# Kernel optimization log

Measured on AMD Instinct MI355X. Metric: run time of the kernel, lower is better.

## Reference

```python
import jax, jax.numpy as jnp
import numpy as np

B, N, D = 32, 256, 3
NF, L = 16, 3


def _fully_connected(n):
    # Same ordering as connect_fully: for i in range(n) for j in range(n) if i != j
    a = np.repeat(np.arange(n), n)
    b = np.tile(np.arange(n), n)
    m = a != b
    return a[m].astype(np.int32), b[m].astype(np.int32)


def setup_inputs() -> dict:
    key = jax.random.key(0)
    ks = jax.random.split(key, 12)
    src, dst = _fully_connected(N)
    s = 0.1  # small param scale for numerical stability
    return {
        "xs": jax.random.normal(ks[0], (B, N, D), jnp.float32),
        "vs": jax.random.normal(ks[1], (B, N, D), jnp.float32),
        "charges": jax.random.normal(ks[2], (B * N, 1), jnp.float32),
        "W_in": s * jax.random.normal(ks[3], (1, NF), jnp.float32),
        "b_in": jnp.zeros((NF,), jnp.float32),
        "W_v": s * jax.random.normal(ks[4], (L, NF, 1), jnp.float32),
        "We1": s * jax.random.normal(ks[5], (L, 2 * NF + 1, NF), jnp.float32),
        "be1": jnp.zeros((L, NF), jnp.float32),
        "We2": s * jax.random.normal(ks[6], (L, NF, NF), jnp.float32),
        "be2": jnp.zeros((L, NF), jnp.float32),
        "Wx": s * jax.random.normal(ks[7], (L, NF, 1), jnp.float32),
        "Wh1": s * jax.random.normal(ks[8], (L, 2 * NF, NF), jnp.float32),
        "bh1": jnp.zeros((L, NF), jnp.float32),
        "src": jnp.asarray(src),
        "dst": jnp.asarray(dst),
    }


def reference(xs, vs, charges, W_in, b_in, W_v, We1, be1, We2, be2, Wx, Wh1, bh1, src, dst):
    b, n, d = xs.shape
    # node scalar features from charges (ndata['f'])
    h = jax.nn.relu(charges.reshape(b, n, 1) @ W_in + b_in)  # [B,N,nf]
    x = xs
    n_layers = We1.shape[0]
    for l in range(n_layers):
        # fully-connected edge gather + subtract (edata['d'])
        de = x[:, dst] - x[:, src]                         # [B,E,3]
        r2 = jnp.sum(de * de, axis=-1, keepdims=True)      # [B,E,1]
        e_in = jnp.concatenate([h[:, src], h[:, dst], r2], axis=-1)  # [B,E,2nf+1]
        m = jax.nn.relu(e_in @ We1[l] + be1[l])
        m = jax.nn.relu(m @ We2[l] + be2[l])               # [B,E,nf]
        w = m @ Wx[l]                                      # [B,E,1]
        # equivariant coordinate update: scatter-add edge vectors into dst nodes
        agg_x = jnp.zeros_like(x).at[:, dst].add(de * w) / (n - 1)
        x = x + agg_x + vs * (h @ W_v[l])                  # velocity term (ndata['vel'])
        m_agg = jnp.zeros_like(h).at[:, dst].add(m)        # [B,N,nf]
        h = h + jax.nn.relu(jnp.concatenate([h, m_agg], axis=-1) @ Wh1[l] + bh1[l])
    # OurDynamics returns (se3_out['1'] + xs).view(-1, n_dimension)
    return x.reshape(-1, d)
```

## Files before the change

kernel.cpp:

```cpp
#include <hip/hip_runtime.h>

#define NN 256
#define NF 16

typedef _Float16 half4 __attribute__((ext_vector_type(4)));
typedef _Float16 h2 __attribute__((ext_vector_type(2)));
typedef __fp16 fh2 __attribute__((ext_vector_type(2)));
typedef float f32x4 __attribute__((ext_vector_type(4)));

#define CVTPK(a, b) __builtin_bit_cast(h2, __builtin_amdgcn_cvt_pkrtz((a), (b)))
#define FDOT2(a, b, c) __builtin_amdgcn_fdot2(__builtin_bit_cast(fh2, (a)), __builtin_bit_cast(fh2, (b)), (c), false)

#define XA_OFF 0
#define XB_OFF 32768
#define HA_OFF 65536
#define HB_OFF 196608
#define SUA_OFF 327680
#define SVA_OFF 458752
#define SUB_OFF 589824
#define SVB_OFF 720896

__global__ __launch_bounds__(256)
void layer0_kernel(const float* __restrict__ xs, const float* __restrict__ vs,
                   const float* __restrict__ charges,
                   const float* __restrict__ W_in, const float* __restrict__ b_in,
                   const float* __restrict__ W_v, const float* __restrict__ We1_l,
                   const float* __restrict__ be1_l, const float* __restrict__ We2_l,
                   const float* __restrict__ be2_l, const float* __restrict__ Wx_l,
                   const float* __restrict__ Wh1_l, const float* __restrict__ bh1_l,
                   const float* __restrict__ We1_n, const float* __restrict__ be1_n,
                   float* __restrict__ x_out, float* __restrict__ h_out,
                   float* __restrict__ su_out, float* __restrict__ sv_out) {
    __shared__ __align__(16) _Float16 sSUh[NN][20];
    __shared__ __align__(16) float sX[NN * 4];
    __shared__ __align__(16) float sHg[64 * NF];
    __shared__ float sWs[256], sWd[256];
    __shared__ __align__(16) float sSV8[8][NF];
    __shared__ __align__(16) float sH8[8][NF + 1];
    __shared__ float sWh1s[512];
    __shared__ float sWa[256], sWb[256];
    __shared__ float sbe1n[NF];
    __shared__ float sh_new[8][NF + 1];
    __shared__ float sg[8][NF];

    const int tid  = threadIdx.x;
    const int b    = blockIdx.x >> 5;
    const int oct  = blockIdx.x & 31;
    const int n0l  = 8 * oct;
    const size_t n0 = (size_t)b * NN + n0l;
    const int w    = tid >> 6;
    const int lane = tid & 63;
    const int c    = lane & 15;
    const int g    = lane >> 4;

    sWs[tid] = We1_l[tid];
    sWd[tid] = We1_l[256 + tid];
    sWh1s[tid]       = Wh1_l[tid];
    sWh1s[256 + tid] = Wh1_l[256 + tid];
    {
        const int f = tid >> 4, kk = tid & 15;
        sWa[kk * NF + f] = We1_n[tid];
        sWb[kk * NF + f] = We1_n[256 + tid];
        if (tid < NF) sbe1n[tid] = be1_n[tid];
    }
    {
        const size_t base = ((size_t)b * NN + tid) * 3;
        const float x0v = xs[base + 0], x1v = xs[base + 1], x2v = xs[base + 2];
        sX[tid * 4 + 0] = x0v;
        sX[tid * 4 + 1] = x1v;
        sX[tid * 4 + 2] = x2v;
        sX[tid * 4 + 3] = fmaf(x0v, x0v, fmaf(x1v, x1v, x2v * x2v));
    }

    const int nl = tid >> 4, k = tid & 15;
    const float win  = W_in[k];
    const float bin  = b_in[k];
    const float be1k = be1_l[k];
    const int i0 = n0l >> 6;
    const int r0 = (n0l & 63) >> 4;
    const int halfsel = (n0l >> 3) & 1;
    const int own = ((nl >> 3) == halfsel);
#pragma unroll
    for (int i = 0; i < 4; ++i) {
#pragma unroll
        for (int r = 0; r < 4; ++r) {
            const float cq = charges[(size_t)b * NN + 64 * i + 16 * r + nl];
            const float hf = fmaxf(fmaf(cq, win, bin), 0.f);
            sHg[(16 * r + nl) * NF + k] = hf;
            if (i == i0 && r == r0 && own) sH8[nl & 7][k] = hf;
        }
        __syncthreads();
#pragma unroll
        for (int r = 0; r < 4; ++r) {
            const float4* hn = (const float4*)&sHg[(16 * r + nl) * NF];
            const float4 h0q = hn[0], h1q = hn[1], h2q = hn[2], h3q = hn[3];
            float u = 0.f;
#pragma unroll
            for (int q = 0; q < 4; ++q) {
                const float4 hq = (q == 0) ? h0q : (q == 1) ? h1q : (q == 2) ? h2q : h3q;
                u = fmaf(hq.x, sWs[(4 * q + 0) * NF + k], u);
                u = fmaf(hq.y, sWs[(4 * q + 1) * NF + k], u);
                u = fmaf(hq.z, sWs[(4 * q + 2) * NF + k], u);
                u = fmaf(hq.w, sWs[(4 * q + 3) * NF + k], u);
            }
            sSUh[64 * i + 16 * r + nl][k] = (_Float16)u;
            if (i == i0 && r == r0 && own) {
                float v = be1k;
#pragma unroll
                for (int q = 0; q < 4; ++q) {
                    const float4 hq = (q == 0) ? h0q : (q == 1) ? h1q : (q == 2) ? h2q : h3q;
                    v = fmaf(hq.x, sWd[(4 * q + 0) * NF + k], v);
                    v = fmaf(hq.y, sWd[(4 * q + 1) * NF + k], v);
                    v = fmaf(hq.z, sWd[(4 * q + 2) * NF + k], v);
                    v = fmaf(hq.w, sWd[(4 * q + 3) * NF + k], v);
                }
                sSV8[nl & 7][k] = v;
            }
        }
        __syncthreads();
    }

    const int j0 = n0l + w, j1 = n0l + 4 + w;
    const float4 xj0 = *(const float4*)&sX[4 * j0];
    const float4 xj1 = *(const float4*)&sX[4 * j1];
    half4 afrag;
    afrag.x = (_Float16)We2_l[(4 * g + 0) * NF + c];
    afrag.y = (_Float16)We2_l[(4 * g + 1) * NF + c];
    afrag.z = (_Float16)We2_l[(4 * g + 2) * NF + c];
    afrag.w = (_Float16)We2_l[(4 * g + 3) * NF + c];
    const float4 v40 = *(const float4*)&sSV8[w][4 * g];
    const float4 v41 = *(const float4*)&sSV8[4 + w][4 * g];
    const float4 wr4  = *(const float4*)(We1_l + 512 + 4 * g);
    const float4 be2f = *(const float4*)(be2_l + 4 * g);
    const float4 wxf  = *(const float4*)(Wx_l + 4 * g);
    f32x4 cb;
    cb.x = be2f.x; cb.y = be2f.y; cb.z = be2f.z; cb.w = be2f.w;
    const h2 wrp01 = CVTPK(wr4.x, wr4.y), wrp23 = CVTPK(wr4.z, wr4.w);
    const h2 vp001 = CVTPK(v40.x, v40.y), vp023 = CVTPK(v40.z, v40.w);
    const h2 vp101 = CVTPK(v41.x, v41.y), vp123 = CVTPK(v41.z, v41.w);
    const h2 wxp01 = CVTPK(wxf.x, wxf.y), wxp23 = CVTPK(wxf.z, wxf.w);
    h2 hz; hz.x = (_Float16)0.f; hz.y = (_Float16)0.f;
    const float m20x = -2.f * xj0.x, m20y = -2.f * xj0.y, m20z = -2.f * xj0.z;
    const float m21x = -2.f * xj1.x, m21y = -2.f * xj1.y, m21z = -2.f * xj1.z;

    float Sw0 = 0.f, Swx0 = 0.f, Swy0 = 0.f, Swz0 = 0.f;
    float Sw1 = 0.f, Swx1 = 0.f, Swy1 = 0.f, Swz1 = 0.f;
    h2 g01_0 = hz, g23_0 = hz, g01_1 = hz, g23_1 = hz;

    const _Float16* su_lh = &sSUh[c][4 * g];
    const float* x_l  = &sX[4 * c];

#pragma unroll 2
    for (int t = 0; t < 16; ++t) {
        const half4 uh = *(const half4*)(su_lh + 320 * t);
        const float4 xs4 = *(const float4*)(x_l + 64 * t);
        h2 u01, u23;
        u01.x = uh.x; u01.y = uh.y; u23.x = uh.z; u23.y = uh.w;
        const int s = 16 * t + c;
        {
            const float r2 = fmaf(m20x, xs4.x, fmaf(m20y, xs4.y, fmaf(m20z, xs4.z, xs4.w + xj0.w)));
            const h2 r2v = CVTPK(r2, r2);
            const h2 m01 = __builtin_elementwise_max(r2v * wrp01 + (u01 + vp001), hz);
            const h2 m23 = __builtin_elementwise_max(r2v * wrp23 + (u23 + vp023), hz);
            half4 bfrag;
            bfrag.x = m01.x; bfrag.y = m01.y; bfrag.z = m23.x; bfrag.w = m23.y;
            const f32x4 acc = __builtin_amdgcn_mfma_f32_16x16x16f16(afrag, bfrag, cb, 0, 0, 0);
            const h2 e01 = __builtin_elementwise_max(CVTPK(acc.x, acc.y), hz);
            const h2 e23 = __builtin_elementwise_max(CVTPK(acc.z, acc.w), hz);
            const float wp = FDOT2(e01, wxp01, FDOT2(e23, wxp23, 0.f));
            const unsigned gm = (s != j0) ? 0x3C003C00u : 0u;
            const h2 gu = __builtin_bit_cast(h2, gm);
            g01_0 = e01 * gu + g01_0;
            g23_0 = e23 * gu + g23_0;
            Sw0 += wp;
            Swx0 = fmaf(wp, xs4.x, Swx0);
            Swy0 = fmaf(wp, xs4.y, Swy0);
            Swz0 = fmaf(wp, xs4.z, Swz0);
        }
        {
            const float r2 = fmaf(m21x, xs4.x, fmaf(m21y, xs4.y, fmaf(m21z, xs4.z, xs4.w + xj1.w)));
            const h2 r2v = CVTPK(r2, r2);
            const h2 m01 = __builtin_elementwise_max(r2v * wrp01 + (u01 + vp101), hz);
            const h2 m23 = __builtin_elementwise_max(r2v * wrp23 + (u23 + vp123), hz);
            half4 bfrag;
            bfrag.x = m01.x; bfrag.y = m01.y; bfrag.z = m23.x; bfrag.w = m23.y;
            const f32x4 acc = __builtin_amdgcn_mfma_f32_16x16x16f16(afrag, bfrag, cb, 0, 0, 0);
            const h2 e01 = __builtin_elementwise_max(CVTPK(acc.x, acc.y), hz);
            const h2 e23 = __builtin_elementwise_max(CVTPK(acc.z, acc.w), hz);
            const float wp = FDOT2(e01, wxp01, FDOT2(e23, wxp23, 0.f));
            const unsigned gm = (s != j1) ? 0x3C003C00u : 0u;
            const h2 gu = __builtin_bit_cast(h2, gm);
            g01_1 = e01 * gu + g01_1;
            g23_1 = e23 * gu + g23_1;
            Sw1 += wp;
            Swx1 = fmaf(wp, xs4.x, Swx1);
            Swy1 = fmaf(wp, xs4.y, Swy1);
            Swz1 = fmaf(wp, xs4.z, Swz1);
        }
    }

#pragma unroll
    for (int off = 1; off < 64; off <<= 1) {
        Sw0  += __shfl_xor(Sw0,  off, 64);  Sw1  += __shfl_xor(Sw1,  off, 64);
        Swx0 += __shfl_xor(Swx0, off, 64);  Swx1 += __shfl_xor(Swx1, off, 64);
        Swy0 += __shfl_xor(Swy0, off, 64);  Swy1 += __shfl_xor(Swy1, off, 64);
        Swz0 += __shfl_xor(Swz0, off, 64);  Swz1 += __shfl_xor(Swz1, off, 64);
    }
#pragma unroll
    for (int off = 1; off < 16; off <<= 1) {
        g01_0 = g01_0 + __builtin_bit_cast(h2, __shfl_xor(__builtin_bit_cast(int, g01_0), off, 64));
        g23_0 = g23_0 + __builtin_bit_cast(h2, __shfl_xor(__builtin_bit_cast(int, g23_0), off, 64));
        g01_1 = g01_1 + __builtin_bit_cast(h2, __shfl_xor(__builtin_bit_cast(int, g01_1), off, 64));
        g23_1 = g23_1 + __builtin_bit_cast(h2, __shfl_xor(__builtin_bit_cast(int, g23_1), off, 64));
    }
    if ((lane & 15) == 0) {
        *(float4*)&sg[w][4 * g]     = make_float4((float)g01_0.x, (float)g01_0.y,
                                                  (float)g23_0.x, (float)g23_0.y);
        *(float4*)&sg[w + 4][4 * g] = make_float4((float)g01_1.x, (float)g01_1.y,
                                                  (float)g23_1.x, (float)g23_1.y);
    }
    __syncthreads();

    const int is0 = (lane < 16);
    const int is1 = (lane >= 32 && lane < 48);
    if (is0 || is1) {
        const int f = lane & 15;
        const int slot = is0 ? w : (w + 4);
        const int jm   = is0 ? j0 : j1;
        const float SwS = is0 ? Sw0  : Sw1;
        const float SxS = is0 ? Swx0 : Swx1;
        const float SyS = is0 ? Swy0 : Swy1;
        const float SzS = is0 ? Swz0 : Swz1;
        const float4 xjm = is0 ? xj0 : xj1;
        const size_t nj = (size_t)b * NN + jm;
        float hd = bh1_l[f];
        float hv = 0.f;
#pragma unroll
        for (int kk = 0; kk < NF; ++kk) {
            const float hjk = sH8[slot][kk];
            hd = fmaf(hjk, sWh1s[kk * NF + f], hd);
            hv = fmaf(hjk, W_v[kk], hv);
        }
#pragma unroll
        for (int kk = 0; kk < NF; ++kk) {
            hd = fmaf(sg[slot][kk], sWh1s[(NF + kk) * NF + f], hd);
        }
        const float hnew = sH8[slot][f] + fmaxf(hd, 0.f);
        sh_new[slot][f] = hnew;
        h_out[nj * NF + f] = hnew;
        if (f < 3) {
            const float xc = (f == 0) ? xjm.x : ((f == 1) ? xjm.y : xjm.z);
            const float Sc = (f == 0) ? SxS  : ((f == 1) ? SyS  : SzS);
            const float agg = (SwS * xc - Sc) * (1.f / 255.f);
            const float xnew = xc + agg + vs[nj * 3 + f] * hv;
            x_out[nj * 4 + f] = xnew;
        }
        if (f == 3) x_out[nj * 4 + 3] = 0.f;
    }

    __syncthreads();
    if (tid < 128) {
        const int jd = tid >> 4, kk = tid & 15;
        float u = 0.f, v = sbe1n[kk];
#pragma unroll
        for (int f = 0; f < NF; ++f) {
            const float hf = sh_new[jd][f];
            u = fmaf(hf, sWa[kk * NF + f], u);
            v = fmaf(hf, sWb[kk * NF + f], v);
        }
        su_out[(n0 + jd) * NF + kk] = u;
        sv_out[(n0 + jd) * NF + kk] = v;
    }
}

__global__ __launch_bounds__(256)
void layer_kernel(const float* __restrict__ x_in, const float* __restrict__ h_in,
                  const float* __restrict__ su_in, const float* __restrict__ sv_in,
                  float* __restrict__ x_out, float* __restrict__ h_out,
                  float* __restrict__ su_out, float* __restrict__ sv_out,
                  const float* __restrict__ vs, const float* __restrict__ Wv_l,
                  const float* __restrict__ We1_l, const float* __restrict__ We2_l,
                  const float* __restrict__ be2_l, const float* __restrict__ Wx_l,
                  const float* __restrict__ Wh1_l, const float* __restrict__ bh1_l,
                  const float* __restrict__ We1_n, const float* __restrict__ be1_n,
                  int final_layer) {
    __shared__ __align__(16) _Float16 sSUh[NN][20];
    __shared__ __align__(16) float sX[NN * 4];
    __shared__ float sWh1s[512];
    __shared__ float sWa[256];
    __shared__ float sWb[256];
    __shared__ float sbe1n[NF];
    __shared__ float sh_new[8][NF + 1];
    __shared__ float sg[8][NF];

    const int tid  = threadIdx.x;
    const int b    = blockIdx.x >> 5;
    const int oct  = blockIdx.x & 31;
    const int n0l  = 8 * oct;
    const size_t n0 = (size_t)b * NN + n0l;
    const int w    = tid >> 6;
    const int lane = tid & 63;
    const int c    = lane & 15;
    const int g    = lane >> 4;

    sWh1s[tid]       = Wh1_l[tid];
    sWh1s[256 + tid] = Wh1_l[256 + tid];
    if (!final_layer) {
        const int f = tid >> 4, k = tid & 15;
        sWa[k * NF + f] = We1_n[tid];
        sWb[k * NF + f] = We1_n[256 + tid];
        if (tid < NF) sbe1n[tid] = be1_n[tid];
    }
    {
        const float4* gsu = (const float4*)(su_in + (size_t)b * NN * NF);
#pragma unroll
        for (int i = 0; i < 4; ++i) {
            const int idx = tid + 256 * i;
            const float4 u = gsu[idx];
            const int node = idx >> 2, k0 = (idx & 3) * 4;
            half4 p;
            p.x = (_Float16)u.x; p.y = (_Float16)u.y;
            p.z = (_Float16)u.z; p.w = (_Float16)u.w;
            *(half4*)&sSUh[node][k0] = p;
        }
        const float4* gx = (const float4*)(x_in + (size_t)b * NN * 4);
        float4 xv = gx[tid];
        xv.w = fmaf(xv.x, xv.x, fmaf(xv.y, xv.y, xv.z * xv.z));
        ((float4*)sX)[tid] = xv;
    }
    __syncthreads();

    const int j0 = n0l + w, j1 = n0l + 4 + w;
    const float4 xj0 = *(const float4*)&sX[4 * j0];
    const float4 xj1 = *(const float4*)&sX[4 * j1];
    half4 afrag;
    afrag.x = (_Float16)We2_l[(4 * g + 0) * NF + c];
    afrag.y = (_Float16)We2_l[(4 * g + 1) * NF + c];
    afrag.z = (_Float16)We2_l[(4 * g + 2) * NF + c];
    afrag.w = (_Float16)We2_l[(4 * g + 3) * NF + c];
    const float4 v40  = *(const float4*)(sv_in + ((size_t)b * NN + j0) * NF + 4 * g);
    const float4 v41  = *(const float4*)(sv_in + ((size_t)b * NN + j1) * NF + 4 * g);
    const float4 wr4  = *(const float4*)(We1_l + 512 + 4 * g);
    const float4 be2f = *(const float4*)(be2_l + 4 * g);
    const float4 wxf  = *(const float4*)(Wx_l + 4 * g);
    f32x4 cb;
    cb.x = be2f.x; cb.y = be2f.y; cb.z = be2f.z; cb.w = be2f.w;
    const h2 wrp01 = CVTPK(wr4.x, wr4.y), wrp23 = CVTPK(wr4.z, wr4.w);
    const h2 vp001 = CVTPK(v40.x, v40.y), vp023 = CVTPK(v40.z, v40.w);
    const h2 vp101 = CVTPK(v41.x, v41.y), vp123 = CVTPK(v41.z, v41.w);
    const h2 wxp01 = CVTPK(wxf.x, wxf.y), wxp23 = CVTPK(wxf.z, wxf.w);
    h2 hz; hz.x = (_Float16)0.f; hz.y = (_Float16)0.f;
    const float m20x = -2.f * xj0.x, m20y = -2.f * xj0.y, m20z = -2.f * xj0.z;
    const float m21x = -2.f * xj1.x, m21y = -2.f * xj1.y, m21z = -2.f * xj1.z;

    float Sw0 = 0.f, Swx0 = 0.f, Swy0 = 0.f, Swz0 = 0.f;
    float Sw1 = 0.f, Swx1 = 0.f, Swy1 = 0.f, Swz1 = 0.f;
    h2 g01_0 = hz, g23_0 = hz, g01_1 = hz, g23_1 = hz;

    const _Float16* su_lh = &sSUh[c][4 * g];
    const float* x_l  = &sX[4 * c];

#pragma unroll 2
    for (int t = 0; t < 16; ++t) {
        const half4 uh = *(const half4*)(su_lh + 320 * t);
        const float4 xs4 = *(const float4*)(x_l + 64 * t);
        h2 u01, u23;
        u01.x = uh.x; u01.y = uh.y; u23.x = uh.z; u23.y = uh.w;
        const int s = 16 * t + c;
        {
            const float r2 = fmaf(m20x, xs4.x, fmaf(m20y, xs4.y, fmaf(m20z, xs4.z, xs4.w + xj0.w)));
            const h2 r2v = CVTPK(r2, r2);
            const h2 m01 = __builtin_elementwise_max(r2v * wrp01 + (u01 + vp001), hz);
            const h2 m23 = __builtin_elementwise_max(r2v * wrp23 + (u23 + vp023), hz);
            half4 bfrag;
            bfrag.x = m01.x; bfrag.y = m01.y; bfrag.z = m23.x; bfrag.w = m23.y;
            const f32x4 acc = __builtin_amdgcn_mfma_f32_16x16x16f16(afrag, bfrag, cb, 0, 0, 0);
            const h2 e01 = __builtin_elementwise_max(CVTPK(acc.x, acc.y), hz);
            const h2 e23 = __builtin_elementwise_max(CVTPK(acc.z, acc.w), hz);
            const float wp = FDOT2(e01, wxp01, FDOT2(e23, wxp23, 0.f));
            const unsigned gm = (s != j0) ? 0x3C003C00u : 0u;
            const h2 gu = __builtin_bit_cast(h2, gm);
            g01_0 = e01 * gu + g01_0;
            g23_0 = e23 * gu + g23_0;
            Sw0 += wp;
            Swx0 = fmaf(wp, xs4.x, Swx0);
            Swy0 = fmaf(wp, xs4.y, Swy0);
            Swz0 = fmaf(wp, xs4.z, Swz0);
        }
        {
            const float r2 = fmaf(m21x, xs4.x, fmaf(m21y, xs4.y, fmaf(m21z, xs4.z, xs4.w + xj1.w)));
            const h2 r2v = CVTPK(r2, r2);
            const h2 m01 = __builtin_elementwise_max(r2v * wrp01 + (u01 + vp101), hz);
            const h2 m23 = __builtin_elementwise_max(r2v * wrp23 + (u23 + vp123), hz);
            half4 bfrag;
            bfrag.x = m01.x; bfrag.y = m01.y; bfrag.z = m23.x; bfrag.w = m23.y;
            const f32x4 acc = __builtin_amdgcn_mfma_f32_16x16x16f16(afrag, bfrag, cb, 0, 0, 0);
            const h2 e01 = __builtin_elementwise_max(CVTPK(acc.x, acc.y), hz);
            const h2 e23 = __builtin_elementwise_max(CVTPK(acc.z, acc.w), hz);
            const float wp = FDOT2(e01, wxp01, FDOT2(e23, wxp23, 0.f));
            const unsigned gm = (s != j1) ? 0x3C003C00u : 0u;
            const h2 gu = __builtin_bit_cast(h2, gm);
            g01_1 = e01 * gu + g01_1;
            g23_1 = e23 * gu + g23_1;
            Sw1 += wp;
            Swx1 = fmaf(wp, xs4.x, Swx1);
            Swy1 = fmaf(wp, xs4.y, Swy1);
            Swz1 = fmaf(wp, xs4.z, Swz1);
        }
    }

#pragma unroll
    for (int off = 1; off < 64; off <<= 1) {
        Sw0  += __shfl_xor(Sw0,  off, 64);  Sw1  += __shfl_xor(Sw1,  off, 64);
        Swx0 += __shfl_xor(Swx0, off, 64);  Swx1 += __shfl_xor(Swx1, off, 64);
        Swy0 += __shfl_xor(Swy0, off, 64);  Swy1 += __shfl_xor(Swy1, off, 64);
        Swz0 += __shfl_xor(Swz0, off, 64);  Swz1 += __shfl_xor(Swz1, off, 64);
    }
#pragma unroll
    for (int off = 1; off < 16; off <<= 1) {
        g01_0 = g01_0 + __builtin_bit_cast(h2, __shfl_xor(__builtin_bit_cast(int, g01_0), off, 64));
        g23_0 = g23_0 + __builtin_bit_cast(h2, __shfl_xor(__builtin_bit_cast(int, g23_0), off, 64));
        g01_1 = g01_1 + __builtin_bit_cast(h2, __shfl_xor(__builtin_bit_cast(int, g01_1), off, 64));
        g23_1 = g23_1 + __builtin_bit_cast(h2, __shfl_xor(__builtin_bit_cast(int, g23_1), off, 64));
    }
    if ((lane & 15) == 0) {
        *(float4*)&sg[w][4 * g]     = make_float4((float)g01_0.x, (float)g01_0.y,
                                                  (float)g23_0.x, (float)g23_0.y);
        *(float4*)&sg[w + 4][4 * g] = make_float4((float)g01_1.x, (float)g01_1.y,
                                                  (float)g23_1.x, (float)g23_1.y);
    }
    __syncthreads();

    const int is0 = (lane < 16);
    const int is1 = (lane >= 32 && lane < 48);
    if (is0 || is1) {
        const int f = lane & 15;
        const int slot = is0 ? w : (w + 4);
        const int jm   = is0 ? j0 : j1;
        const float SwS = is0 ? Sw0  : Sw1;
        const float SxS = is0 ? Swx0 : Swx1;
        const float SyS = is0 ? Swy0 : Swy1;
        const float SzS = is0 ? Swz0 : Swz1;
        const float4 xjm = is0 ? xj0 : xj1;
        const size_t nj = (size_t)b * NN + jm;
        float hd = bh1_l[f];
        float hv = 0.f;
#pragma unroll
        for (int k = 0; k < NF; ++k) {
            const float hjk = h_in[nj * NF + k];
            hd = fmaf(hjk, sWh1s[k * NF + f], hd);
            hv = fmaf(hjk, Wv_l[k], hv);
        }
#pragma unroll
        for (int k = 0; k < NF; ++k) {
            hd = fmaf(sg[slot][k], sWh1s[(NF + k) * NF + f], hd);
        }
        const float hnew = h_in[nj * NF + f] + fmaxf(hd, 0.f);
        sh_new[slot][f] = hnew;
        if (!final_layer) h_out[nj * NF + f] = hnew;
        if (f < 3) {
            const float xc = (f == 0) ? xjm.x : ((f == 1) ? xjm.y : xjm.z);
            const float Sc = (f == 0) ? SxS  : ((f == 1) ? SyS  : SzS);
            const float agg = (SwS * xc - Sc) * (1.f / 255.f);
            const float xnew = xc + agg + vs[nj * 3 + f] * hv;
            if (final_layer) x_out[nj * 3 + f] = xnew;
            else             x_out[nj * 4 + f] = xnew;
        }
        if (!final_layer && f == 3) x_out[nj * 4 + 3] = 0.f;
    }

    if (!final_layer) {
        __syncthreads();
        if (tid < 128) {
            const int jd = tid >> 4, k = tid & 15;
            float u = 0.f, v = sbe1n[k];
#pragma unroll
            for (int f = 0; f < NF; ++f) {
                const float hf = sh_new[jd][f];
                u = fmaf(hf, sWa[k * NF + f], u);
                v = fmaf(hf, sWb[k * NF + f], v);
            }
            su_out[(n0 + jd) * NF + k] = u;
            sv_out[(n0 + jd) * NF + k] = v;
        }
    }
}

extern "C" void kernel_launch(void* const* d_in, const int* in_sizes, int n_in,
                              void* d_out, int out_size, void* d_ws, size_t ws_size,
                              hipStream_t stream) {
    const float* xs      = (const float*)d_in[0];
    const float* vs      = (const float*)d_in[1];
    const float* charges = (const float*)d_in[2];
    const float* W_in    = (const float*)d_in[3];
    const float* b_in    = (const float*)d_in[4];
    const float* W_v     = (const float*)d_in[5];
    const float* We1     = (const float*)d_in[6];
    const float* be1     = (const float*)d_in[7];
    const float* We2     = (const float*)d_in[8];
    const float* be2     = (const float*)d_in[9];
    const float* Wx      = (const float*)d_in[10];
    const float* Wh1     = (const float*)d_in[11];
    const float* bh1     = (const float*)d_in[12];

    float* ws = (float*)d_ws;
    float* xA  = ws + XA_OFF;
    float* xB  = ws + XB_OFF;
    float* hA  = ws + HA_OFF;
    float* hB  = ws + HB_OFF;
    float* suA = ws + SUA_OFF;
    float* svA = ws + SVA_OFF;
    float* suB = ws + SUB_OFF;
    float* svB = ws + SVB_OFF;
    float* out = (float*)d_out;

    hipLaunchKernelGGL(layer0_kernel, dim3(1024), dim3(256), 0, stream,
                       xs, vs, charges, W_in, b_in,
                       W_v + 0 * 16, We1 + 0 * 528, be1 + 0 * 16, We2 + 0 * 256,
                       be2 + 0 * 16, Wx + 0 * 16, Wh1 + 0 * 512, bh1 + 0 * 16,
                       We1 + 1 * 528, be1 + 1 * 16,
                       xA, hA, suA, svA);
    hipLaunchKernelGGL(layer_kernel, dim3(1024), dim3(256), 0, stream,
                       xA, hA, suA, svA, xB, hB, suB, svB,
                       vs, W_v + 1 * 16, We1 + 1 * 528, We2 + 1 * 256,
                       be2 + 1 * 16, Wx + 1 * 16, Wh1 + 1 * 512, bh1 + 1 * 16,
                       We1 + 2 * 528, be1 + 2 * 16, 0);
    hipLaunchKernelGGL(layer_kernel, dim3(1024), dim3(256), 0, stream,
                       xB, hB, suB, svB, out, hA, suA, svA,
                       vs, W_v + 2 * 16, We1 + 2 * 528, We2 + 2 * 256,
                       be2 + 2 * 16, Wx + 2 * 16, Wh1 + 2 * 512, bh1 + 2 * 16,
                       We1 + 2 * 528, be1 + 2 * 16, 1);
}
```

Measured before the change: 126.4 us.

## Split source-node loop across two waves per target pair with 512-thread blocks

Doubles the block size to 512 threads so each pair of target nodes is handled by two waves, each covering half of the 256 source nodes. Partial message sums and coordinate weight sums are written to shared memory per half and combined in the node-update phase, which now uses one wave per target node. The aim is more latency hiding and shorter per-wave loops on the edge stage. The cost is extra shared-memory reductions and a tighter register budget from the 512,8 launch bounds.

```diff
diff --git a/kernel.cpp b/kernel.cpp
--- a/kernel.cpp
+++ b/kernel.cpp
@@ -20,7 +20,7 @@
 #define SUB_OFF 589824
 #define SVB_OFF 720896
 
-__global__ __launch_bounds__(256)
+__global__ __launch_bounds__(512, 8)
 void layer0_kernel(const float* __restrict__ xs, const float* __restrict__ vs,
                    const float* __restrict__ charges,
                    const float* __restrict__ W_in, const float* __restrict__ b_in,
@@ -41,7 +41,8 @@
     __shared__ float sWa[256], sWb[256];
     __shared__ float sbe1n[NF];
     __shared__ float sh_new[8][NF + 1];
-    __shared__ float sg[8][NF];
+    __shared__ __align__(16) float sg2[2][8][NF];
+    __shared__ __align__(16) float sSw[2][8][4];
 
     const int tid  = threadIdx.x;
     const int b    = blockIdx.x >> 5;
@@ -49,21 +50,24 @@
     const int n0l  = 8 * oct;
     const size_t n0 = (size_t)b * NN + n0l;
     const int w    = tid >> 6;
+    const int p    = w >> 1;
+    const int hh   = w & 1;
     const int lane = tid & 63;
     const int c    = lane & 15;
     const int g    = lane >> 4;
 
-    sWs[tid] = We1_l[tid];
-    sWd[tid] = We1_l[256 + tid];
-    sWh1s[tid]       = Wh1_l[tid];
-    sWh1s[256 + tid] = Wh1_l[256 + tid];
-    {
+    if (tid < 256) {
+        sWs[tid] = We1_l[tid];
+        sWd[tid] = We1_l[256 + tid];
+    }
+    sWh1s[tid] = Wh1_l[tid];
+    if (tid < 256) {
         const int f = tid >> 4, kk = tid & 15;
         sWa[kk * NF + f] = We1_n[tid];
         sWb[kk * NF + f] = We1_n[256 + tid];
         if (tid < NF) sbe1n[tid] = be1_n[tid];
     }
-    {
+    if (tid < 256) {
         const size_t base = ((size_t)b * NN + tid) * 3;
         const float x0v = xs[base + 0], x1v = xs[base + 1], x2v = xs[base + 2];
         sX[tid * 4 + 0] = x0v;
@@ -72,7 +76,7 @@
         sX[tid * 4 + 3] = fmaf(x0v, x0v, fmaf(x1v, x1v, x2v * x2v));
     }
 
-    const int nl = tid >> 4, k = tid & 15;
+    const int nl = (tid >> 4) & 15, k = tid & 15;
     const float win  = W_in[k];
     const float bin  = b_in[k];
     const float be1k = be1_l[k];
@@ -82,45 +86,49 @@
     const int own = ((nl >> 3) == halfsel);
 #pragma unroll
     for (int i = 0; i < 4; ++i) {
-#pragma unroll
-        for (int r = 0; r < 4; ++r) {
-            const float cq = charges[(size_t)b * NN + 64 * i + 16 * r + nl];
-            const float hf = fmaxf(fmaf(cq, win, bin), 0.f);
-            sHg[(16 * r + nl) * NF + k] = hf;
-            if (i == i0 && r == r0 && own) sH8[nl & 7][k] = hf;
+        if (tid < 256) {
+#pragma unroll
+            for (int r = 0; r < 4; ++r) {
+                const float cq = charges[(size_t)b * NN + 64 * i + 16 * r + nl];
+                const float hf = fmaxf(fmaf(cq, win, bin), 0.f);
+                sHg[(16 * r + nl) * NF + k] = hf;
+                if (i == i0 && r == r0 && own) sH8[nl & 7][k] = hf;
+            }
         }
         __syncthreads();
-#pragma unroll
-        for (int r = 0; r < 4; ++r) {
-            const float4* hn = (const float4*)&sHg[(16 * r + nl) * NF];
-            const float4 h0q = hn[0], h1q = hn[1], h2q = hn[2], h3q = hn[3];
-            float u = 0.f;
-#pragma unroll
-            for (int q = 0; q < 4; ++q) {
-                const float4 hq = (q == 0) ? h0q : (q == 1) ? h1q : (q == 2) ? h2q : h3q;
-                u = fmaf(hq.x, sWs[(4 * q + 0) * NF + k], u);
-                u = fmaf(hq.y, sWs[(4 * q + 1) * NF + k], u);
-                u = fmaf(hq.z, sWs[(4 * q + 2) * NF + k], u);
-                u = fmaf(hq.w, sWs[(4 * q + 3) * NF + k], u);
-            }
-            sSUh[64 * i + 16 * r + nl][k] = (_Float16)u;
-            if (i == i0 && r == r0 && own) {
-                float v = be1k;
+        if (tid < 256) {
+#pragma unroll
+            for (int r = 0; r < 4; ++r) {
+                const float4* hn = (const float4*)&sHg[(16 * r + nl) * NF];
+                const float4 h0q = hn[0], h1q = hn[1], h2q = hn[2], h3q = hn[3];
+                float u = 0.f;
 #pragma unroll
                 for (int q = 0; q < 4; ++q) {
                     const float4 hq = (q == 0) ? h0q : (q == 1) ? h1q : (q == 2) ? h2q : h3q;
-                    v = fmaf(hq.x, sWd[(4 * q + 0) * NF + k], v);
-                    v = fmaf(hq.y, sWd[(4 * q + 1) * NF + k], v);
-                    v = fmaf(hq.z, sWd[(4 * q + 2) * NF + k], v);
-                    v = fmaf(hq.w, sWd[(4 * q + 3) * NF + k], v);
+                    u = fmaf(hq.x, sWs[(4 * q + 0) * NF + k], u);
+                    u = fmaf(hq.y, sWs[(4 * q + 1) * NF + k], u);
+                    u = fmaf(hq.z, sWs[(4 * q + 2) * NF + k], u);
+                    u = fmaf(hq.w, sWs[(4 * q + 3) * NF + k], u);
                 }
-                sSV8[nl & 7][k] = v;
+                sSUh[64 * i + 16 * r + nl][k] = (_Float16)u;
+                if (i == i0 && r == r0 && own) {
+                    float v = be1k;
+#pragma unroll
+                    for (int q = 0; q < 4; ++q) {
+                        const float4 hq = (q == 0) ? h0q : (q == 1) ? h1q : (q == 2) ? h2q : h3q;
+                        v = fmaf(hq.x, sWd[(4 * q + 0) * NF + k], v);
+                        v = fmaf(hq.y, sWd[(4 * q + 1) * NF + k], v);
+                        v = fmaf(hq.z, sWd[(4 * q + 2) * NF + k], v);
+                        v = fmaf(hq.w, sWd[(4 * q + 3) * NF + k], v);
+                    }
+                    sSV8[nl & 7][k] = v;
+                }
             }
         }
         __syncthreads();
     }
 
-    const int j0 = n0l + w, j1 = n0l + 4 + w;
+    const int j0 = n0l + p, j1 = n0l + 4 + p;
     const float4 xj0 = *(const float4*)&sX[4 * j0];
     const float4 xj1 = *(const float4*)&sX[4 * j1];
     half4 afrag;
@@ -128,8 +136,8 @@
     afrag.y = (_Float16)We2_l[(4 * g + 1) * NF + c];
     afrag.z = (_Float16)We2_l[(4 * g + 2) * NF + c];
     afrag.w = (_Float16)We2_l[(4 * g + 3) * NF + c];
-    const float4 v40 = *(const float4*)&sSV8[w][4 * g];
-    const float4 v41 = *(const float4*)&sSV8[4 + w][4 * g];
+    const float4 v40 = *(const float4*)&sSV8[p][4 * g];
+    const float4 v41 = *(const float4*)&sSV8[4 + p][4 * g];
     const float4 wr4  = *(const float4*)(We1_l + 512 + 4 * g);
     const float4 be2f = *(const float4*)(be2_l + 4 * g);
     const float4 wxf  = *(const float4*)(Wx_l + 4 * g);
@@ -149,9 +157,10 @@
 
     const _Float16* su_lh = &sSUh[c][4 * g];
     const float* x_l  = &sX[4 * c];
+    const int t0 = 8 * hh;
 
 #pragma unroll 2
-    for (int t = 0; t < 16; ++t) {
+    for (int t = t0; t < t0 + 8; ++t) {
         const half4 uh = *(const half4*)(su_lh + 320 * t);
         const float4 xs4 = *(const float4*)(x_l + 64 * t);
         h2 u01, u23;
@@ -214,39 +223,40 @@
         g23_1 = g23_1 + __builtin_bit_cast(h2, __shfl_xor(__builtin_bit_cast(int, g23_1), off, 64));
     }
     if ((lane & 15) == 0) {
-        *(float4*)&sg[w][4 * g]     = make_float4((float)g01_0.x, (float)g01_0.y,
-                                                  (float)g23_0.x, (float)g23_0.y);
-        *(float4*)&sg[w + 4][4 * g] = make_float4((float)g01_1.x, (float)g01_1.y,
-                                                  (float)g23_1.x, (float)g23_1.y);
+        *(float4*)&sg2[hh][p][4 * g]     = make_float4((float)g01_0.x, (float)g01_0.y,
+                                                       (float)g23_0.x, (float)g23_0.y);
+        *(float4*)&sg2[hh][p + 4][4 * g] = make_float4((float)g01_1.x, (float)g01_1.y,
+                                                       (float)g23_1.x, (float)g23_1.y);
+    }
+    if (lane == 0) {
+        *(float4*)&sSw[hh][p][0]     = make_float4(Sw0, Swx0, Swy0, Swz0);
+        *(float4*)&sSw[hh][p + 4][0] = make_float4(Sw1, Swx1, Swy1, Swz1);
     }
     __syncthreads();
 
-    const int is0 = (lane < 16);
-    const int is1 = (lane >= 32 && lane < 48);
-    if (is0 || is1) {
-        const int f = lane & 15;
-        const int slot = is0 ? w : (w + 4);
-        const int jm   = is0 ? j0 : j1;
-        const float SwS = is0 ? Sw0  : Sw1;
-        const float SxS = is0 ? Swx0 : Swx1;
-        const float SyS = is0 ? Swy0 : Swy1;
-        const float SzS = is0 ? Swz0 : Swz1;
-        const float4 xjm = is0 ? xj0 : xj1;
+    if (lane < 16) {
+        const int f = lane;
+        const int jm = n0l + w;
         const size_t nj = (size_t)b * NN + jm;
+        const float SwS = sSw[0][w][0] + sSw[1][w][0];
+        const float SxS = sSw[0][w][1] + sSw[1][w][1];
+        const float SyS = sSw[0][w][2] + sSw[1][w][2];
+        const float SzS = sSw[0][w][3] + sSw[1][w][3];
+        const float4 xjm = *(const float4*)&sX[4 * jm];
         float hd = bh1_l[f];
         float hv = 0.f;
 #pragma unroll
         for (int kk = 0; kk < NF; ++kk) {
-            const float hjk = sH8[slot][kk];
+            const float hjk = sH8[w][kk];
             hd = fmaf(hjk, sWh1s[kk * NF + f], hd);
             hv = fmaf(hjk, W_v[kk], hv);
         }
 #pragma unroll
         for (int kk = 0; kk < NF; ++kk) {
-            hd = fmaf(sg[slot][kk], sWh1s[(NF + kk) * NF + f], hd);
-        }
-        const float hnew = sH8[slot][f] + fmaxf(hd, 0.f);
-        sh_new[slot][f] = hnew;
+            hd = fmaf(sg2[0][w][kk] + sg2[1][w][kk], sWh1s[(NF + kk) * NF + f], hd);
+        }
+        const float hnew = sH8[w][f] + fmaxf(hd, 0.f);
+        sh_new[w][f] = hnew;
         h_out[nj * NF + f] = hnew;
         if (f < 3) {
             const float xc = (f == 0) ? xjm.x : ((f == 1) ? xjm.y : xjm.z);
@@ -273,7 +283,7 @@
     }
 }
 
-__global__ __launch_bounds__(256)
+__global__ __launch_bounds__(512, 8)
 void layer_kernel(const float* __restrict__ x_in, const float* __restrict__ h_in,
                   const float* __restrict__ su_in, const float* __restrict__ sv_in,
                   float* __restrict__ x_out, float* __restrict__ h_out,
@@ -291,7 +301,8 @@
     __shared__ float sWb[256];
     __shared__ float sbe1n[NF];
     __shared__ float sh_new[8][NF + 1];
-    __shared__ float sg[8][NF];
+    __shared__ __align__(16) float sg2[2][8][NF];
+    __shared__ __align__(16) float sSw[2][8][4];
 
     const int tid  = threadIdx.x;
     const int b    = blockIdx.x >> 5;
@@ -299,13 +310,14 @@
     const int n0l  = 8 * oct;
     const size_t n0 = (size_t)b * NN + n0l;
     const int w    = tid >> 6;
+    const int p    = w >> 1;
+    const int hh   = w & 1;
     const int lane = tid & 63;
     const int c    = lane & 15;
     const int g    = lane >> 4;
 
-    sWh1s[tid]       = Wh1_l[tid];
-    sWh1s[256 + tid] = Wh1_l[256 + tid];
-    if (!final_layer) {
+    sWh1s[tid] = Wh1_l[tid];
+    if (!final_layer && tid < 256) {
         const int f = tid >> 4, k = tid & 15;
         sWa[k * NF + f] = We1_n[tid];
         sWb[k * NF + f] = We1_n[256 + tid];
@@ -314,23 +326,25 @@
     {
         const float4* gsu = (const float4*)(su_in + (size_t)b * NN * NF);
 #pragma unroll
-        for (int i = 0; i < 4; ++i) {
-            const int idx = tid + 256 * i;
+        for (int i = 0; i < 2; ++i) {
+            const int idx = tid + 512 * i;
             const float4 u = gsu[idx];
             const int node = idx >> 2, k0 = (idx & 3) * 4;
-            half4 p;
-            p.x = (_Float16)u.x; p.y = (_Float16)u.y;
-            p.z = (_Float16)u.z; p.w = (_Float16)u.w;
-            *(half4*)&sSUh[node][k0] = p;
-        }
-        const float4* gx = (const float4*)(x_in + (size_t)b * NN * 4);
-        float4 xv = gx[tid];
-        xv.w = fmaf(xv.x, xv.x, fmaf(xv.y, xv.y, xv.z * xv.z));
-        ((float4*)sX)[tid] = xv;
+            half4 pk;
+            pk.x = (_Float16)u.x; pk.y = (_Float16)u.y;
+            pk.z = (_Float16)u.z; pk.w = (_Float16)u.w;
+            *(half4*)&sSUh[node][k0] = pk;
+        }
+        if (tid < 256) {
+            const float4* gx = (const float4*)(x_in + (size_t)b * NN * 4);
+            float4 xv = gx[tid];
+            xv.w = fmaf(xv.x, xv.x, fmaf(xv.y, xv.y, xv.z * xv.z));
+            ((float4*)sX)[tid] = xv;
+        }
     }
     __syncthreads();
 
-    const int j0 = n0l + w, j1 = n0l + 4 + w;
+    const int j0 = n0l + p, j1 = n0l + 4 + p;
     const float4 xj0 = *(const float4*)&sX[4 * j0];
     const float4 xj1 = *(const float4*)&sX[4 * j1];
     half4 afrag;
@@ -359,9 +373,10 @@
 
     const _Float16* su_lh = &sSUh[c][4 * g];
     const float* x_l  = &sX[4 * c];
+    const int t0 = 8 * hh;
 
 #pragma unroll 2
-    for (int t = 0; t < 16; ++t) {
+    for (int t = t0; t < t0 + 8; ++t) {
         const half4 uh = *(const half4*)(su_lh + 320 * t);
         const float4 xs4 = *(const float4*)(x_l + 64 * t);
         h2 u01, u23;
@@ -424,25 +439,26 @@
         g23_1 = g23_1 + __builtin_bit_cast(h2, __shfl_xor(__builtin_bit_cast(int, g23_1), off, 64));
     }
     if ((lane & 15) == 0) {
-        *(float4*)&sg[w][4 * g]     = make_float4((float)g01_0.x, (float)g01_0.y,
-                                                  (float)g23_0.x, (float)g23_0.y);
-        *(float4*)&sg[w + 4][4 * g] = make_float4((float)g01_1.x, (float)g01_1.y,
-                                                  (float)g23_1.x, (float)g23_1.y);
+        *(float4*)&sg2[hh][p][4 * g]     = make_float4((float)g01_0.x, (float)g01_0.y,
+                                                       (float)g23_0.x, (float)g23_0.y);
+        *(float4*)&sg2[hh][p + 4][4 * g] = make_float4((float)g01_1.x, (float)g01_1.y,
+                                                       (float)g23_1.x, (float)g23_1.y);
+    }
+    if (lane == 0) {
+        *(float4*)&sSw[hh][p][0]     = make_float4(Sw0, Swx0, Swy0, Swz0);
+        *(float4*)&sSw[hh][p + 4][0] = make_float4(Sw1, Swx1, Swy1, Swz1);
     }
     __syncthreads();
 
-    const int is0 = (lane < 16);
-    const int is1 = (lane >= 32 && lane < 48);
-    if (is0 || is1) {
-        const int f = lane & 15;
-        const int slot = is0 ? w : (w + 4);
-        const int jm   = is0 ? j0 : j1;
-        const float SwS = is0 ? Sw0  : Sw1;
-        const float SxS = is0 ? Swx0 : Swx1;
-        const float SyS = is0 ? Swy0 : Swy1;
-        const float SzS = is0 ? Swz0 : Swz1;
-        const float4 xjm = is0 ? xj0 : xj1;
+    if (lane < 16) {
+        const int f = lane;
+        const int jm = n0l + w;
         const size_t nj = (size_t)b * NN + jm;
+        const float SwS = sSw[0][w][0] + sSw[1][w][0];
+        const float SxS = sSw[0][w][1] + sSw[1][w][1];
+        const float SyS = sSw[0][w][2] + sSw[1][w][2];
+        const float SzS = sSw[0][w][3] + sSw[1][w][3];
+        const float4 xjm = *(const float4*)&sX[4 * jm];
         float hd = bh1_l[f];
         float hv = 0.f;
 #pragma unroll
@@ -453,10 +469,10 @@
         }
 #pragma unroll
         for (int k = 0; k < NF; ++k) {
-            hd = fmaf(sg[slot][k], sWh1s[(NF + k) * NF + f], hd);
+            hd = fmaf(sg2[0][w][k] + sg2[1][w][k], sWh1s[(NF + k) * NF + f], hd);
         }
         const float hnew = h_in[nj * NF + f] + fmaxf(hd, 0.f);
-        sh_new[slot][f] = hnew;
+        sh_new[w][f] = hnew;
         if (!final_layer) h_out[nj * NF + f] = hnew;
         if (f < 3) {
             const float xc = (f == 0) ? xjm.x : ((f == 1) ? xjm.y : xjm.z);
@@ -514,18 +530,18 @@
     float* svB = ws + SVB_OFF;
     float* out = (float*)d_out;
 
-    hipLaunchKernelGGL(layer0_kernel, dim3(1024), dim3(256), 0, stream,
+    hipLaunchKernelGGL(layer0_kernel, dim3(1024), dim3(512), 0, stream,
                        xs, vs, charges, W_in, b_in,
                        W_v + 0 * 16, We1 + 0 * 528, be1 + 0 * 16, We2 + 0 * 256,
                        be2 + 0 * 16, Wx + 0 * 16, Wh1 + 0 * 512, bh1 + 0 * 16,
                        We1 + 1 * 528, be1 + 1 * 16,
                        xA, hA, suA, svA);
-    hipLaunchKernelGGL(layer_kernel, dim3(1024), dim3(256), 0, stream,
+    hipLaunchKernelGGL(layer_kernel, dim3(1024), dim3(512), 0, stream,
                        xA, hA, suA, svA, xB, hB, suB, svB,
                        vs, W_v + 1 * 16, We1 + 1 * 528, We2 + 1 * 256,
                        be2 + 1 * 16, Wx + 1 * 16, Wh1 + 1 * 512, bh1 + 1 * 16,
                        We1 + 2 * 528, be1 + 2 * 16, 0);
-    hipLaunchKernelGGL(layer_kernel, dim3(1024), dim3(256), 0, stream,
+    hipLaunchKernelGGL(layer_kernel, dim3(1024), dim3(512), 0, stream,
                        xB, hB, suB, svB, out, hA, suA, svA,
                        vs, W_v + 2 * 16, We1 + 2 * 528, We2 + 2 * 256,
                        be2 + 2 * 16, Wx + 2 * 16, Wh1 + 2 * 512, bh1 + 2 * 16,
```

New measurement: 135.3 us. 7.1% more time.
